# Kernel tuning notes

Hardware: AMD Instinct MI355X
Metric: run time of the kernel (lower is better)

## Reference

```python
import jax, jax.numpy as jnp
import numpy as np

COMMITMENT_COST = 0.25
CODE_BOOK_SIZE = 1024
EMBED_DIM = 64


def setup_inputs() -> dict:
    key = jax.random.key(0)
    k1, k2 = jax.random.split(key)
    inputs = jax.random.normal(k1, (32, 64, 32, 32), dtype=jnp.float32)
    # matches torch init: uniform(-1/K, 1/K)
    embedding = jax.random.uniform(
        k2, (CODE_BOOK_SIZE, EMBED_DIM), dtype=jnp.float32,
        minval=-1.0 / CODE_BOOK_SIZE, maxval=1.0 / CODE_BOOK_SIZE)
    return {"inputs": inputs, "embedding": embedding}


def reference(inputs, embedding):
    # inputs: [B, D, H, W] -> [B, H, W, D]
    x = jnp.transpose(inputs, (0, 2, 3, 1))
    B, H, W, D = x.shape
    flat = x.reshape(-1, D)                                   # [N, D]
    # ((x - e)**2).mean(-1), without the [N, K, D] broadcast tensor)
    x2 = jnp.sum(flat * flat, axis=1, keepdims=True)          # [N, 1]
    e2 = jnp.sum(embedding * embedding, axis=1)               # [K]
    distances = (x2 - 2.0 * (flat @ embedding.T) + e2) / D    # [N, K]
    encoding_indices = jnp.argmin(distances, axis=1)          # [N]
    quantized = embedding[encoding_indices].reshape(B, H, W, D)
    e_latent_loss = jnp.mean((jax.lax.stop_gradient(quantized) - x) ** 2)
    q_latent_loss = jnp.mean((quantized - jax.lax.stop_gradient(x)) ** 2)
    loss = q_latent_loss + COMMITMENT_COST * e_latent_loss
    # straight-through estimator (training mode); value identical to quantized
    quantized = x + jax.lax.stop_gradient(quantized - x)
    return (loss,
            jnp.transpose(quantized, (0, 3, 1, 2)),
            encoding_indices.reshape(B, -1))
```

## Files before the change

kernel.cpp:

```cpp
#include <hip/hip_runtime.h>


constexpr int D_   = 64;
constexpr int HW   = 1024;
constexpr int K_   = 1024;
constexpr int PTS  = 64;
constexpr int SP   = 68;
constexpr int SEK  = 516;
constexpr int QE   = 2097152;
constexpr int IDX_OFF = 1 + QE;

__global__ __launch_bounds__(256, 2) void vq_main_kernel(
    const float* __restrict__ in, const float* __restrict__ emb,
    float* __restrict__ out, float* __restrict__ loss_acc,
    unsigned* __restrict__ cnt) {
  __shared__ float xT[D_ * SP];
  __shared__ float eTs[16 * SEK];
  __shared__ float e2s[K_];
  __shared__ float x2s[PTS];
  __shared__ int   idx_sel[PTS];
  __shared__ float redbuf[4];

  const int t   = threadIdx.x;
  const int kg  = t & 31;
  const int ptg = t >> 5;
  const int blk = blockIdx.x;
  const int b   = blk >> 4;
  const int hw0 = (blk & 15) * PTS;
  const float* inb = in + b * (D_ * HW) + hw0;

#pragma unroll
  for (int i = 0; i < 4; ++i) {
    int fi = t + i * 256;
    int d  = fi >> 4, p4 = fi & 15;
    *(float4*)(&xT[d * SP + p4 * 4]) = *(const float4*)(inb + d * HW + p4 * 4);
  }

#pragma unroll
  for (int c = 0; c < 4; ++c) {
    int k = t + c * 256;
    const float4* e4 = (const float4*)(emb + k * 64);
    float s = 0.f;
#pragma unroll
    for (int q = 0; q < 16; ++q) {
      float4 v = e4[q];
      s += v.x * v.x; s += v.y * v.y; s += v.z * v.z; s += v.w * v.w;
    }
    e2s[k] = s;
  }
  __syncthreads();

  if (t < PTS) {
    float s = 0.f;
#pragma unroll 8
    for (int d = 0; d < D_; ++d) { float xv = xT[d * SP + t]; s = fmaf(xv, xv, s); }
    x2s[t] = s;
  }
  __syncthreads();

  float x2r[8];
  {
    float4 xa = *(const float4*)&x2s[ptg * 8];
    float4 xb = *(const float4*)&x2s[ptg * 8 + 4];
    x2r[0]=xa.x; x2r[1]=xa.y; x2r[2]=xa.z; x2r[3]=xa.w;
    x2r[4]=xb.x; x2r[5]=xb.y; x2r[6]=xb.z; x2r[7]=xb.w;
  }

  int eoff[4];
#pragma unroll
  for (int q = 0; q < 4; ++q)
    eoff[q] = 4 * (((kg + q) & 7) + 8 * ((kg >> 3) + 4 * q));

  float minv[8]; int mini[8];
#pragma unroll
  for (int i = 0; i < 8; ++i) { minv[i] = 3.4e38f; mini[i] = 0; }

#pragma unroll 1
  for (int pass = 0; pass < 2; ++pass) {
    float acc[8][16];
#pragma unroll
    for (int i = 0; i < 8; ++i)
#pragma unroll
      for (int j = 0; j < 16; ++j) acc[i][j] = 0.f;

#pragma unroll 1
    for (int s = 0; s < 4; ++s) {
      __syncthreads();
      {
        int c0 = 2 * t;
        int kgs = c0 >> 4, qs = (c0 >> 2) & 3, js = c0 & 3;
        int Cc = 4 * (((kgs + qs) & 7) + 8 * ((kgs >> 3) + 4 * qs)) + js;
        const float4* ga = (const float4*)(emb + (pass * 512 + c0) * 64 + s * 16);
        const float4* gb = (const float4*)(emb + (pass * 512 + c0 + 1) * 64 + s * 16);
        float4 a[4], bb[4];
#pragma unroll
        for (int r = 0; r < 4; ++r) { a[r] = ga[r]; bb[r] = gb[r]; }
#pragma unroll
        for (int r = 0; r < 4; ++r) {
          float av[4] = {a[r].x, a[r].y, a[r].z, a[r].w};
          float bv[4] = {bb[r].x, bb[r].y, bb[r].z, bb[r].w};
#pragma unroll
          for (int jd = 0; jd < 4; ++jd)
            *(float2*)(&eTs[(r * 4 + jd) * SEK + Cc]) = make_float2(av[jd], bv[jd]);
        }
      }
      __syncthreads();

#pragma unroll 4
      for (int dd = 0; dd < 16; ++dd) {
        int drow = dd * SEK;
        int dg   = s * 16 + dd;
        float4 xa = *(const float4*)&xT[dg * SP + ptg * 8];
        float4 xb = *(const float4*)&xT[dg * SP + ptg * 8 + 4];
        float4 e0 = *(const float4*)&eTs[drow + eoff[0]];
        float4 e1 = *(const float4*)&eTs[drow + eoff[1]];
        float4 e2 = *(const float4*)&eTs[drow + eoff[2]];
        float4 e3 = *(const float4*)&eTs[drow + eoff[3]];
        float xf[8]  = {xa.x, xa.y, xa.z, xa.w, xb.x, xb.y, xb.z, xb.w};
        float ef[16] = {e0.x, e0.y, e0.z, e0.w, e1.x, e1.y, e1.z, e1.w,
                        e2.x, e2.y, e2.z, e2.w, e3.x, e3.y, e3.z, e3.w};
#pragma unroll
        for (int i = 0; i < 8; ++i)
#pragma unroll
          for (int j = 0; j < 16; ++j)
            acc[i][j] = fmaf(xf[i], ef[j], acc[i][j]);
      }
    }

    float e2f[16];
    {
      const float4* p4 = (const float4*)&e2s[pass * 512 + kg * 16];
#pragma unroll
      for (int q = 0; q < 4; ++q) {
        float4 v = p4[q];
        e2f[q*4+0]=v.x; e2f[q*4+1]=v.y; e2f[q*4+2]=v.z; e2f[q*4+3]=v.w;
      }
    }
#pragma unroll
    for (int j = 0; j < 16; ++j) {
      int cg = pass * 512 + kg * 16 + j;
      float e2v = e2f[j];
#pragma unroll
      for (int i = 0; i < 8; ++i) {
        float u = fmaf(-2.f, acc[i][j], x2r[i]) + e2v;
        if (u < minv[i]) { minv[i] = u; mini[i] = cg; }
      }
    }
  }

#pragma unroll
  for (int i = 0; i < 8; ++i) {
    float v = minv[i]; int ix = mini[i];
#pragma unroll
    for (int off = 1; off < 32; off <<= 1) {
      float vo = __shfl_xor(v, off);
      int   io = __shfl_xor(ix, off);
      if (vo < v || (vo == v && io < ix)) { v = vo; ix = io; }
    }
    if (kg == 0) idx_sel[ptg * 8 + i] = ix;
  }
  __syncthreads();

  if (t < PTS) out[IDX_OFF + blk * PTS + t] = (float)idx_sel[t];

  float lp = 0.f;
#pragma unroll
  for (int i = 0; i < 4; ++i) {
    int fi = t + i * 256;
    int p = fi & 63, qd = fi >> 6;
    int cidx = idx_sel[p];
    float4 q = *(const float4*)(emb + cidx * 64 + qd * 4);
    float xv0 = xT[(qd * 4 + 0) * SP + p];
    float xv1 = xT[(qd * 4 + 1) * SP + p];
    float xv2 = xT[(qd * 4 + 2) * SP + p];
    float xv3 = xT[(qd * 4 + 3) * SP + p];
    float d0 = q.x - xv0, d1 = q.y - xv1, d2 = q.z - xv2, d3 = q.w - xv3;
    lp = fmaf(d0, d0, lp); lp = fmaf(d1, d1, lp);
    lp = fmaf(d2, d2, lp); lp = fmaf(d3, d3, lp);
    xT[(qd * 4 + 0) * SP + p] = xv0 + d0;
    xT[(qd * 4 + 1) * SP + p] = xv1 + d1;
    xT[(qd * 4 + 2) * SP + p] = xv2 + d2;
    xT[(qd * 4 + 3) * SP + p] = xv3 + d3;
  }

#pragma unroll
  for (int off = 1; off < 64; off <<= 1) lp += __shfl_xor(lp, off);
  if ((t & 63) == 0) redbuf[t >> 6] = lp;
  __syncthreads();
  if (t == 0) {
    atomicAdd(loss_acc, redbuf[0] + redbuf[1] + redbuf[2] + redbuf[3]);
    __threadfence();
    unsigned old = atomicAdd(cnt, 1u);
    if (old == 511u) {
      __threadfence();
      float total = atomicAdd(loss_acc, 0.0f);
      float m = total * (1.0f / 2097152.0f);
      out[0] = m + 0.25f * m;
    }
  }

  float* outq = out + 1 + b * (D_ * HW) + hw0;
#pragma unroll
  for (int i = 0; i < 16; ++i) {
    int oi = t + i * 256;
    int d = oi >> 6, p = oi & 63;
    outq[d * HW + p] = xT[d * SP + p];
  }
}

extern "C" void kernel_launch(void* const* d_in, const int* in_sizes, int n_in,
                              void* d_out, int out_size, void* d_ws, size_t ws_size,
                              hipStream_t stream) {
  const float* in  = (const float*)d_in[0];
  const float* emb = (const float*)d_in[1];
  float* out = (float*)d_out;
  float* loss_acc = (float*)d_ws;
  unsigned* cnt   = (unsigned*)d_ws + 4;

  hipMemsetAsync(d_ws, 0, 64, stream);
  vq_main_kernel<<<512, 256, 0, stream>>>(in, emb, out, loss_acc, cnt);
}
```

Baseline: 148.9 us.

## Enlarge point tile and register-prefetch full-depth codebook chunks

Each block now covers 128 points with 512 threads. The codebook is staged in chunks of 256 codes at full depth D=64 instead of 16-deep slices. The next chunk is prefetched into registers while the current one is consumed, which cuts the number of barriers and stage-copy overheads. The per-thread tile shrinks from 8x16 to 8x8 accumulators, and the grid is halved to 256 blocks. This lowers arithmetic intensity per thread and may leave CUs underfilled on a 256-CU device.

```diff
diff --git a/kernel.cpp b/kernel.cpp
--- a/kernel.cpp
+++ b/kernel.cpp
@@ -4,41 +4,45 @@
 constexpr int D_   = 64;
 constexpr int HW   = 1024;
 constexpr int K_   = 1024;
-constexpr int PTS  = 64;
-constexpr int SP   = 68;
-constexpr int SEK  = 516;
+constexpr int PTS  = 128;
+constexpr int SP   = 132;
+constexpr int SEC  = 260;
+constexpr int CK   = 256;
 constexpr int QE   = 2097152;
 constexpr int IDX_OFF = 1 + QE;
 
-__global__ __launch_bounds__(256, 2) void vq_main_kernel(
+__global__ __launch_bounds__(512, 2) void vq_main_kernel(
     const float* __restrict__ in, const float* __restrict__ emb,
     float* __restrict__ out, float* __restrict__ loss_acc,
     unsigned* __restrict__ cnt) {
   __shared__ float xT[D_ * SP];
-  __shared__ float eTs[16 * SEK];
+  __shared__ float eTs[D_ * SEC];
   __shared__ float e2s[K_];
   __shared__ float x2s[PTS];
   __shared__ int   idx_sel[PTS];
-  __shared__ float redbuf[4];
+  __shared__ float redbuf[8];
 
   const int t   = threadIdx.x;
   const int kg  = t & 31;
   const int ptg = t >> 5;
   const int blk = blockIdx.x;
-  const int b   = blk >> 4;
-  const int hw0 = (blk & 15) * PTS;
+  const int b   = blk >> 3;
+  const int hw0 = (blk & 7) * PTS;
   const float* inb = in + b * (D_ * HW) + hw0;
 
+  const int kl = t >> 1;
+  const int h  = t & 1;
+
 #pragma unroll
   for (int i = 0; i < 4; ++i) {
-    int fi = t + i * 256;
-    int d  = fi >> 4, p4 = fi & 15;
+    int fi = t + i * 512;
+    int d  = fi >> 5, p4 = fi & 31;
     *(float4*)(&xT[d * SP + p4 * 4]) = *(const float4*)(inb + d * HW + p4 * 4);
   }
 
 #pragma unroll
-  for (int c = 0; c < 4; ++c) {
-    int k = t + c * 256;
+  for (int c = 0; c < 2; ++c) {
+    int k = t + c * 512;
     const float4* e4 = (const float4*)(emb + k * 64);
     float s = 0.f;
 #pragma unroll
@@ -47,6 +51,21 @@
       s += v.x * v.x; s += v.y * v.y; s += v.z * v.z; s += v.w * v.w;
     }
     e2s[k] = s;
+  }
+
+  float4 pf[8];
+  {
+    const float4* g = (const float4*)(emb + kl * 64 + h * 32);
+#pragma unroll
+    for (int r = 0; r < 8; ++r) pf[r] = g[r];
+#pragma unroll
+    for (int r = 0; r < 8; ++r) {
+      int d = h * 32 + r * 4;
+      eTs[(d + 0) * SEC + kl] = pf[r].x;
+      eTs[(d + 1) * SEC + kl] = pf[r].y;
+      eTs[(d + 2) * SEC + kl] = pf[r].z;
+      eTs[(d + 3) * SEC + kl] = pf[r].w;
+    }
   }
   __syncthreads();
 
@@ -66,79 +85,49 @@
     x2r[4]=xb.x; x2r[5]=xb.y; x2r[6]=xb.z; x2r[7]=xb.w;
   }
 
-  int eoff[4];
-#pragma unroll
-  for (int q = 0; q < 4; ++q)
-    eoff[q] = 4 * (((kg + q) & 7) + 8 * ((kg >> 3) + 4 * q));
-
   float minv[8]; int mini[8];
 #pragma unroll
   for (int i = 0; i < 8; ++i) { minv[i] = 3.4e38f; mini[i] = 0; }
 
 #pragma unroll 1
-  for (int pass = 0; pass < 2; ++pass) {
-    float acc[8][16];
+  for (int c = 0; c < 4; ++c) {
+    if (c < 3) {
+      const float4* g = (const float4*)(emb + ((c + 1) * CK + kl) * 64 + h * 32);
+#pragma unroll
+      for (int r = 0; r < 8; ++r) pf[r] = g[r];
+    }
+
+    float acc[8][8];
 #pragma unroll
     for (int i = 0; i < 8; ++i)
 #pragma unroll
-      for (int j = 0; j < 16; ++j) acc[i][j] = 0.f;
-
-#pragma unroll 1
-    for (int s = 0; s < 4; ++s) {
-      __syncthreads();
-      {
-        int c0 = 2 * t;
-        int kgs = c0 >> 4, qs = (c0 >> 2) & 3, js = c0 & 3;
-        int Cc = 4 * (((kgs + qs) & 7) + 8 * ((kgs >> 3) + 4 * qs)) + js;
-        const float4* ga = (const float4*)(emb + (pass * 512 + c0) * 64 + s * 16);
-        const float4* gb = (const float4*)(emb + (pass * 512 + c0 + 1) * 64 + s * 16);
-        float4 a[4], bb[4];
-#pragma unroll
-        for (int r = 0; r < 4; ++r) { a[r] = ga[r]; bb[r] = gb[r]; }
-#pragma unroll
-        for (int r = 0; r < 4; ++r) {
-          float av[4] = {a[r].x, a[r].y, a[r].z, a[r].w};
-          float bv[4] = {bb[r].x, bb[r].y, bb[r].z, bb[r].w};
-#pragma unroll
-          for (int jd = 0; jd < 4; ++jd)
-            *(float2*)(&eTs[(r * 4 + jd) * SEK + Cc]) = make_float2(av[jd], bv[jd]);
-        }
-      }
-      __syncthreads();
-
-#pragma unroll 4
-      for (int dd = 0; dd < 16; ++dd) {
-        int drow = dd * SEK;
-        int dg   = s * 16 + dd;
-        float4 xa = *(const float4*)&xT[dg * SP + ptg * 8];
-        float4 xb = *(const float4*)&xT[dg * SP + ptg * 8 + 4];
-        float4 e0 = *(const float4*)&eTs[drow + eoff[0]];
-        float4 e1 = *(const float4*)&eTs[drow + eoff[1]];
-        float4 e2 = *(const float4*)&eTs[drow + eoff[2]];
-        float4 e3 = *(const float4*)&eTs[drow + eoff[3]];
-        float xf[8]  = {xa.x, xa.y, xa.z, xa.w, xb.x, xb.y, xb.z, xb.w};
-        float ef[16] = {e0.x, e0.y, e0.z, e0.w, e1.x, e1.y, e1.z, e1.w,
-                        e2.x, e2.y, e2.z, e2.w, e3.x, e3.y, e3.z, e3.w};
-#pragma unroll
-        for (int i = 0; i < 8; ++i)
-#pragma unroll
-          for (int j = 0; j < 16; ++j)
-            acc[i][j] = fmaf(xf[i], ef[j], acc[i][j]);
-      }
-    }
-
-    float e2f[16];
+      for (int j = 0; j < 8; ++j) acc[i][j] = 0.f;
+
+#pragma unroll 2
+    for (int d = 0; d < D_; ++d) {
+      float4 xa = *(const float4*)&xT[d * SP + ptg * 8];
+      float4 xb = *(const float4*)&xT[d * SP + ptg * 8 + 4];
+      float4 e0 = *(const float4*)&eTs[d * SEC + kg * 8];
+      float4 e1 = *(const float4*)&eTs[d * SEC + kg * 8 + 4];
+      float xf[8] = {xa.x, xa.y, xa.z, xa.w, xb.x, xb.y, xb.z, xb.w};
+      float ef[8] = {e0.x, e0.y, e0.z, e0.w, e1.x, e1.y, e1.z, e1.w};
+#pragma unroll
+      for (int i = 0; i < 8; ++i)
+#pragma unroll
+        for (int j = 0; j < 8; ++j)
+          acc[i][j] = fmaf(xf[i], ef[j], acc[i][j]);
+    }
+
+    float e2f[8];
     {
-      const float4* p4 = (const float4*)&e2s[pass * 512 + kg * 16];
-#pragma unroll
-      for (int q = 0; q < 4; ++q) {
-        float4 v = p4[q];
-        e2f[q*4+0]=v.x; e2f[q*4+1]=v.y; e2f[q*4+2]=v.z; e2f[q*4+3]=v.w;
-      }
-    }
-#pragma unroll
-    for (int j = 0; j < 16; ++j) {
-      int cg = pass * 512 + kg * 16 + j;
+      const float4* p4 = (const float4*)&e2s[c * CK + kg * 8];
+      float4 v0 = p4[0], v1 = p4[1];
+      e2f[0]=v0.x; e2f[1]=v0.y; e2f[2]=v0.z; e2f[3]=v0.w;
+      e2f[4]=v1.x; e2f[5]=v1.y; e2f[6]=v1.z; e2f[7]=v1.w;
+    }
+#pragma unroll
+    for (int j = 0; j < 8; ++j) {
+      int cg = c * CK + kg * 8 + j;
       float e2v = e2f[j];
 #pragma unroll
       for (int i = 0; i < 8; ++i) {
@@ -146,6 +135,19 @@
         if (u < minv[i]) { minv[i] = u; mini[i] = cg; }
       }
     }
+
+    if (c < 3) {
+      __syncthreads();
+#pragma unroll
+      for (int r = 0; r < 8; ++r) {
+        int d = h * 32 + r * 4;
+        eTs[(d + 0) * SEC + kl] = pf[r].x;
+        eTs[(d + 1) * SEC + kl] = pf[r].y;
+        eTs[(d + 2) * SEC + kl] = pf[r].z;
+        eTs[(d + 3) * SEC + kl] = pf[r].w;
+      }
+      __syncthreads();
+    }
   }
 
 #pragma unroll
@@ -166,8 +168,8 @@
   float lp = 0.f;
 #pragma unroll
   for (int i = 0; i < 4; ++i) {
-    int fi = t + i * 256;
-    int p = fi & 63, qd = fi >> 6;
+    int fi = t + i * 512;
+    int p = fi & 127, qd = fi >> 7;
     int cidx = idx_sel[p];
     float4 q = *(const float4*)(emb + cidx * 64 + qd * 4);
     float xv0 = xT[(qd * 4 + 0) * SP + p];
@@ -188,10 +190,13 @@
   if ((t & 63) == 0) redbuf[t >> 6] = lp;
   __syncthreads();
   if (t == 0) {
-    atomicAdd(loss_acc, redbuf[0] + redbuf[1] + redbuf[2] + redbuf[3]);
+    float part = 0.f;
+#pragma unroll
+    for (int w = 0; w < 8; ++w) part += redbuf[w];
+    atomicAdd(loss_acc, part);
     __threadfence();
     unsigned old = atomicAdd(cnt, 1u);
-    if (old == 511u) {
+    if (old == 255u) {
       __threadfence();
       float total = atomicAdd(loss_acc, 0.0f);
       float m = total * (1.0f / 2097152.0f);
@@ -202,8 +207,8 @@
   float* outq = out + 1 + b * (D_ * HW) + hw0;
 #pragma unroll
   for (int i = 0; i < 16; ++i) {
-    int oi = t + i * 256;
-    int d = oi >> 6, p = oi & 63;
+    int oi = t + i * 512;
+    int d = oi >> 7, p = oi & 127;
     outq[d * HW + p] = xT[d * SP + p];
   }
 }
@@ -218,5 +223,5 @@
   unsigned* cnt   = (unsigned*)d_ws + 4;
 
   hipMemsetAsync(d_ws, 0, 64, stream);
-  vq_main_kernel<<<512, 256, 0, stream>>>(in, emb, out, loss_acc, cnt);
+  vq_main_kernel<<<256, 512, 0, stream>>>(in, emb, out, loss_acc, cnt);
 }
```

Result: faster. 138.9 us (-6.7%).
